# Kernel tuning notes

Hardware: AMD Instinct MI355X
Metric: run time of the kernel (lower is better)

The kernel has to match this reference:

```python
import jax, jax.numpy as jnp
import numpy as np

N = 50000
E = 800000
D = 128
NUM_GRAPHS = 64
NEG_SLOPE = 0.2


def _gat_conv(x, src, dst, W, a_src, a_dst, bias):
    """PyG GATConv with heads=1, concat=True. src/dst include self-loops."""
    h = x @ W                                  # [N, D_out]
    alpha_s = h @ a_src                        # [N]
    alpha_d = h @ a_dst                        # [N]
    e = alpha_s[src] + alpha_d[dst]            # [E_tot] edge scores
    e = jnp.where(e > 0, e, NEG_SLOPE * e)     # LeakyReLU(0.2)
    # numerically-stable softmax over incoming edges of each dst node
    m = jax.ops.segment_max(e, dst, num_segments=N)
    m = jnp.where(jnp.isfinite(m), m, 0.0)
    ex = jnp.exp(e - m[dst])
    s = jax.ops.segment_sum(ex, dst, num_segments=N)
    coef = ex / (s[dst] + 1e-16)               # [E_tot]
    msg = h[src] * coef[:, None]               # [E_tot, D_out] gathered messages
    out = jax.ops.segment_sum(msg, dst, num_segments=N)
    return out + bias


def setup_inputs() -> dict:
    key = jax.random.key(0)
    ks = jax.random.split(key, 12)
    x = jax.random.normal(ks[0], (N, D), dtype=jnp.float32)
    edge_index = jax.random.randint(ks[1], (2, E), 0, N, dtype=jnp.int64)
    batch = jnp.sort(jax.random.randint(ks[2], (N,), 0, NUM_GRAPHS, dtype=jnp.int64))
    g = 1.0 / np.sqrt(D)
    W1 = jax.random.normal(ks[3], (D, D), dtype=jnp.float32) * g
    as1 = jax.random.normal(ks[4], (D,), dtype=jnp.float32) * g
    ad1 = jax.random.normal(ks[5], (D,), dtype=jnp.float32) * g
    b1 = jnp.zeros((D,), dtype=jnp.float32)
    W2 = jax.random.normal(ks[6], (D, D), dtype=jnp.float32) * g
    as2 = jax.random.normal(ks[7], (D,), dtype=jnp.float32) * g
    ad2 = jax.random.normal(ks[8], (D,), dtype=jnp.float32) * g
    b2 = jnp.zeros((D,), dtype=jnp.float32)
    return {"x": x, "edge_index": edge_index, "batch": batch,
            "W1": W1, "as1": as1, "ad1": ad1, "b1": b1,
            "W2": W2, "as2": as2, "ad2": ad2, "b2": b2}


def reference(x, edge_index, batch, W1, as1, ad1, b1, W2, as2, ad2, b2):
    # PyG GATConv adds self-loops by default
    loops = jnp.arange(N, dtype=edge_index.dtype)
    src = jnp.concatenate([edge_index[0], loops])
    dst = jnp.concatenate([edge_index[1], loops])
    feats = _gat_conv(x, src, dst, W1, as1, ad1, b1)
    feats = _gat_conv(feats, src, dst, W2, as2, ad2, b2)
    # global mean pool over graphs in the batch
    sums = jax.ops.segment_sum(feats, batch, num_segments=NUM_GRAPHS)
    counts = jax.ops.segment_sum(jnp.ones((N,), feats.dtype), batch, num_segments=NUM_GRAPHS)
    pooled = sums / jnp.maximum(counts, 1.0)[:, None]
    return feats, pooled
```

## Files before the change

### kernel.cpp

```cpp
#include <hip/hip_runtime.h>

#define NN 50000
#define NE 800000
#define DIM 128
#define NG 64
#define ETOT (NE + NN)
#define NEG_SLOPE 0.2f
#define PB 200
#define MAXLG 8
#define NSH 8
#define SHW ((NN + NSH - 1) / NSH)
#define NB_SCAN ((NN + 255) / 256)

typedef unsigned int uint32;
typedef unsigned short ushort;
typedef short bf16x8 __attribute__((ext_vector_type(8)));
typedef float f32x4 __attribute__((ext_vector_type(4)));

static __device__ __forceinline__ uint32 f2bf_pack(float lo, float hi) {
  uint32 a = __float_as_uint(lo), b = __float_as_uint(hi);
  a = (a + 0x7fffu + ((a >> 16) & 1u)) >> 16;
  b = (b + 0x7fffu + ((b >> 16) & 1u)) >> 16;
  return a | (b << 16);
}
static __device__ __forceinline__ ushort f2bf1(float x) {
  uint32 a = __float_as_uint(x);
  a = (a + 0x7fffu + ((a >> 16) & 1u)) >> 16;
  return (ushort)a;
}
static __device__ __forceinline__ float bf_lo(uint32 u) { return __uint_as_float(u << 16); }
static __device__ __forceinline__ float bf_hi(uint32 u) { return __uint_as_float(u & 0xffff0000u); }


__global__ __launch_bounds__(256) void k_init(const float* __restrict__ W1, const float* __restrict__ W2,
                                              ushort* __restrict__ wt1, ushort* __restrict__ wt2,
                                              int* deg, int* fill, float* pooled, float* cnt) {
  int i = blockIdx.x * 256 + threadIdx.x;
  if (i < NN) { deg[i] = 1; fill[i] = 1; }
  if (i < NG * DIM) pooled[i] = 0.f;
  if (i < NG) cnt[i] = 0.f;
  if (i < DIM * DIM) {
    int n = i >> 7, k = i & 127;
    wt1[i] = f2bf1(W1[k * DIM + n]);
    wt2[i] = f2bf1(W2[k * DIM + n]);
  }
}

__global__ __launch_bounds__(256) void k_count(const int* __restrict__ dst, int* __restrict__ deg) {
  int e = blockIdx.x * 256 + threadIdx.x;
  if (e < NE) atomicAdd(&deg[dst[e]], 1);
}


__global__ __launch_bounds__(256) void k_scan1(const int* __restrict__ deg, int* __restrict__ offs,
                                               int* __restrict__ bsum) {
  __shared__ int ws[4];
  const int i = blockIdx.x * 256 + threadIdx.x;
  const int lane = threadIdx.x & 63, wid = threadIdx.x >> 6;
  int x = (i < NN) ? deg[i] : 0;
#pragma unroll
  for (int off = 1; off < 64; off <<= 1) {
    int t = __shfl_up(x, off, 64);
    if (lane >= off) x += t;
  }
  if (lane == 63) ws[wid] = x;
  __syncthreads();
  int pre = 0;
#pragma unroll
  for (int j = 0; j < 3; ++j) if (j < wid) pre += ws[j];
  x += pre;
  if (i < NN) offs[i + 1] = x;
  if (threadIdx.x == 255) bsum[blockIdx.x] = x;
}

__global__ __launch_bounds__(256) void k_scan2(const int* __restrict__ bsum, int* __restrict__ bpre) {
  __shared__ int ws[4];
  const int b = threadIdx.x;
  const int lane = b & 63, wid = b >> 6;
  int v = (b < NB_SCAN) ? bsum[b] : 0;
  int x = v;
#pragma unroll
  for (int off = 1; off < 64; off <<= 1) {
    int t = __shfl_up(x, off, 64);
    if (lane >= off) x += t;
  }
  if (lane == 63) ws[wid] = x;
  __syncthreads();
  int pre = 0;
#pragma unroll
  for (int j = 0; j < 3; ++j) if (j < wid) pre += ws[j];
  x += pre;
  if (b < NB_SCAN) bpre[b] = x - v;
}

__global__ __launch_bounds__(256) void k_scan3(int* __restrict__ offs, const int* __restrict__ bpre) {
  const int i = blockIdx.x * 256 + threadIdx.x;
  if (i < NN) offs[i + 1] += bpre[blockIdx.x];
  if (i == 0) offs[0] = 0;
}

__global__ __launch_bounds__(256) void k_selfloop(const int* __restrict__ offs, int* __restrict__ csr) {
  int i = blockIdx.x * 256 + threadIdx.x;
  if (i < NN) csr[offs[i]] = i;
}

__global__ __launch_bounds__(256) void k_scatter(const int* __restrict__ src, const int* __restrict__ dst,
                                                 const int* __restrict__ offs, int* __restrict__ fill,
                                                 int* __restrict__ csr) {
  const int r = blockIdx.x & (NSH - 1);
  const int bi = blockIdx.x >> 3;
  const int nb = gridDim.x >> 3;
  const int lo = r * SHW, hi = min(lo + SHW, NN);
  for (int e = bi * 256 + threadIdx.x; e < NE; e += nb * 256) {
    int d = dst[e];
    if (d >= lo && d < hi) {
      int p = offs[d] + atomicAdd(&fill[d], 1);
      csr[p] = src[e];
    }
  }
}


template <int A16>
__global__ __launch_bounds__(256) void k_mm(const void* __restrict__ Xv, const ushort* __restrict__ WT,
                                            const float* __restrict__ a_s, const float* __restrict__ a_d,
                                            uint32* __restrict__ H16,
                                            float* __restrict__ alpha_s, float* __restrict__ alpha_d, int n) {
  __shared__ __align__(16) ushort sWT[DIM * DIM];
  __shared__ __align__(16) ushort sA[64 * DIM];
  const int tid = threadIdx.x;
  const int row0 = blockIdx.x * 64;

  {
    const int nr = tid >> 1, h2 = tid & 1;
    const uint4* wp = (const uint4*)(WT + nr * DIM + h2 * 64);
#pragma unroll
    for (int i = 0; i < 8; ++i) {
      uint4 v = wp[i];
      int byte = nr * 256 + (((h2 * 128 + i * 16)) ^ ((nr & 7) << 4));
      *(uint4*)((char*)sWT + byte) = v;
    }
  }
  {
    const int r = tid >> 2, q = tid & 3;
    int rg = row0 + r; if (rg > n - 1) rg = n - 1;
    if (A16) {
      const uint4* xp = (const uint4*)((const uint32*)Xv + (size_t)rg * 64 + q * 16);
#pragma unroll
      for (int i = 0; i < 4; ++i) {
        uint4 pk = xp[i];
        int byte = r * 256 + ((q * 64 + i * 16) ^ ((r & 7) << 4));
        *(uint4*)((char*)sA + byte) = pk;
      }
    } else {
      const float4* xp = (const float4*)((const float*)Xv + (size_t)rg * DIM + q * 32);
#pragma unroll
      for (int i = 0; i < 4; ++i) {
        float4 v0 = xp[2 * i], v1 = xp[2 * i + 1];
        uint4 pk = make_uint4(f2bf_pack(v0.x, v0.y), f2bf_pack(v0.z, v0.w),
                              f2bf_pack(v1.x, v1.y), f2bf_pack(v1.z, v1.w));
        int byte = r * 256 + ((q * 64 + i * 16) ^ ((r & 7) << 4));
        *(uint4*)((char*)sA + byte) = pk;
      }
    }
  }
  __syncthreads();

  const int l = tid & 63, wv = tid >> 6;
  const int jr = l & 15, g = l >> 4;
  const int m0 = wv * 16;
  f32x4 acc[8];
#pragma unroll
  for (int nt = 0; nt < 8; ++nt) acc[nt] = (f32x4){0.f, 0.f, 0.f, 0.f};

  const int ra = m0 + jr;
  const int abase = ra * 256, aswz = (ra & 7) << 4;
  const int bswz = (jr & 7) << 4;
#pragma unroll
  for (int kk = 0; kk < 4; ++kk) {
    const int kb = kk * 64 + g * 16;
    bf16x8 af = *(const bf16x8*)((const char*)sA + abase + (kb ^ aswz));
#pragma unroll
    for (int nt = 0; nt < 8; ++nt) {
      bf16x8 bfg = *(const bf16x8*)((const char*)sWT + (nt * 16 + jr) * 256 + (kb ^ bswz));
      acc[nt] = __builtin_amdgcn_mfma_f32_16x16x32_bf16(af, bfg, acc[nt], 0, 0, 0);
    }
  }

  float asv[8], adv[8];
#pragma unroll
  for (int nt = 0; nt < 8; ++nt) { asv[nt] = a_s[nt * 16 + jr]; adv[nt] = a_d[nt * 16 + jr]; }
#pragma unroll
  for (int j = 0; j < 4; ++j) {
    float ps = 0.f, pd = 0.f;
#pragma unroll
    for (int nt = 0; nt < 8; ++nt) {
      ps = fmaf(acc[nt][j], asv[nt], ps);
      pd = fmaf(acc[nt][j], adv[nt], pd);
    }
#pragma unroll
    for (int off = 1; off < 16; off <<= 1) {
      ps += __shfl_xor(ps, off, 64);
      pd += __shfl_xor(pd, off, 64);
    }
    int r = row0 + m0 + g * 4 + j;
    if (jr == 0 && r < n) { alpha_s[r] = ps; alpha_d[r] = pd; }
  }

  ushort* sOut = sA;
#pragma unroll
  for (int nt = 0; nt < 8; ++nt)
#pragma unroll
    for (int j = 0; j < 4; ++j)
      sOut[(m0 + g * 4 + j) * DIM + nt * 16 + jr] = f2bf1(acc[nt][j]);
#pragma unroll
  for (int i = 0; i < 4; ++i) {
    int r = row0 + m0 + (l >> 4) + i * 4;
    uint4 v = *(const uint4*)((const char*)sOut + m0 * 256 + l * 16 + i * 1024);
    if (r < n) *(uint4*)(H16 + (size_t)(row0 + m0) * 64 + l * 4 + i * 256) = v;
  }
}


#define GATHER4(J)                                                          \
  { int s0 = __shfl(sv, g32 + (J), 64), s1 = __shfl(sv, g32 + (J) + 1, 64), \
        s2 = __shfl(sv, g32 + (J) + 2, 64), s3 = __shfl(sv, g32 + (J) + 3, 64); \
    float c0 = __shfl(ex, g32 + (J), 64), c1 = __shfl(ex, g32 + (J) + 1, 64), \
          c2 = __shfl(ex, g32 + (J) + 2, 64), c3 = __shfl(ex, g32 + (J) + 3, 64); \
    uint32 v0 = H16[(size_t)s0 * 64 + u0];                                  \
    uint32 v1 = H16[(size_t)s1 * 64 + u0];                                  \
    uint32 v2 = H16[(size_t)s2 * 64 + u0];                                  \
    uint32 v3 = H16[(size_t)s3 * 64 + u0];                                  \
    ax = fmaf(c0, bf_lo(v0), ax); ay = fmaf(c0, bf_hi(v0), ay);             \
    ax = fmaf(c1, bf_lo(v1), ax); ay = fmaf(c1, bf_hi(v1), ay);             \
    ax = fmaf(c2, bf_lo(v2), ax); ay = fmaf(c2, bf_hi(v2), ay);             \
    ax = fmaf(c3, bf_lo(v3), ax); ay = fmaf(c3, bf_hi(v3), ay); }

#define GATHER1(J)                                                          \
  { int s0 = __shfl(sv, g32 + (J), 64); float c0 = __shfl(ex, g32 + (J), 64); \
    uint32 v0 = H16[(size_t)s0 * 64 + u0];                                  \
    ax = fmaf(c0, bf_lo(v0), ax); ay = fmaf(c0, bf_hi(v0), ay); }

template <int STORE16>
__global__ __launch_bounds__(256) void k_sm_aggr2(const int* __restrict__ offs, const int* __restrict__ csr,
                                                  const float* __restrict__ alpha_s, const float* __restrict__ alpha_d,
                                                  const uint32* __restrict__ H16, const float* __restrict__ bias,
                                                  float* __restrict__ out, uint32* __restrict__ out16) {
  const int b = blockIdx.x;
  const int half = b & 1;
  const int l = threadIdx.x & 63;
  const int sl = l & 31, g = l >> 5, g32 = g * 32;
  const int pair = (b >> 1) * 4 + (threadIdx.x >> 6);
  const int node = pair * 2 + g;
  const int bg = offs[node], eg = offs[node + 1];
  const int dg = eg - bg;
  const float ad = alpha_d[node];
  const int u0 = half * 32 + sl;

  const int maxd = max(dg, __shfl_xor(dg, 32, 64));
  float ax = 0.f, ay = 0.f, ssum = 0.f;

  if (maxd <= 32) {
    int sv = 0; float sc = -1e30f;
    if (sl < dg) {
      sv = csr[bg + sl];
      sc = alpha_s[sv] + ad;
      sc = sc > 0.f ? sc : NEG_SLOPE * sc;
    }
    float m = sc;
#pragma unroll
    for (int off = 1; off < 32; off <<= 1) m = fmaxf(m, __shfl_xor(m, off, 64));
    float ex = (sl < dg) ? __expf(sc - m) : 0.f;
    ssum = ex;
    int j = 0;
    for (; j + 3 < maxd; j += 4) GATHER4(j);
    for (; j < maxd; ++j) GATHER1(j);
  } else {
    float m = -1e30f;
    for (int j = sl; j < dg; j += 32) {
      float sc = alpha_s[csr[bg + j]] + ad;
      sc = sc > 0.f ? sc : NEG_SLOPE * sc;
      m = fmaxf(m, sc);
    }
#pragma unroll
    for (int off = 1; off < 32; off <<= 1) m = fmaxf(m, __shfl_xor(m, off, 64));
    const int nch = (maxd + 31) >> 5;
    for (int c = 0; c < nch; ++c) {
      int j = c * 32 + sl;
      int sv = 0; float ex = 0.f;
      if (j < dg) {
        sv = csr[bg + j];
        float sc = alpha_s[sv] + ad;
        sc = sc > 0.f ? sc : NEG_SLOPE * sc;
        ex = __expf(sc - m);
      }
      ssum += ex;
      int cnt = min(32, maxd - c * 32);
      int jj = 0;
      for (; jj + 3 < cnt; jj += 4) GATHER4(jj);
      for (; jj < cnt; ++jj) GATHER1(jj);
    }
  }

#pragma unroll
  for (int off = 1; off < 32; off <<= 1) ssum += __shfl_xor(ssum, off, 64);
  const float inv = 1.f / (ssum + 1e-16f);
  const float2 bb = *(const float2*)(bias + 2 * u0);
  const float ox = ax * inv + bb.x, oy = ay * inv + bb.y;
  if (STORE16) {
    out16[(size_t)node * 64 + u0] = f2bf_pack(ox, oy);
  } else {
    *(float2*)(out + (size_t)node * DIM + 2 * u0) = make_float2(ox, oy);
  }
}


__global__ __launch_bounds__(256) void k_pool_partial(const float* __restrict__ feats,
                                                      const int* __restrict__ batch,
                                                      float* __restrict__ pooled, float* __restrict__ cnt) {
  __shared__ float acc[4][MAXLG][DIM];
  __shared__ float lcnt[4][MAXLG];
  const int tid = threadIdx.x;
  const int wid = tid >> 6, l = tid & 63;
  for (int i = tid; i < 4 * MAXLG * DIM; i += 256) ((float*)acc)[i] = 0.f;
  if (tid < 4 * MAXLG) ((float*)lcnt)[tid] = 0.f;
  __syncthreads();

  const int chunk = (NN + PB - 1) / PB;
  const int beg = blockIdx.x * chunk;
  const int end = min(beg + chunk, NN);
  const int g0 = (beg < NN) ? batch[beg] : 0;

  for (int node = beg + wid; node < end; node += 4) {
    int lg = batch[node] - g0;
    float2 v = *(const float2*)(feats + (size_t)node * DIM + 2 * l);
    if (lg < MAXLG) {
      acc[wid][lg][2 * l] += v.x;
      acc[wid][lg][2 * l + 1] += v.y;
      if (l == 0) lcnt[wid][lg] += 1.f;
    } else {
      atomicAdd(&pooled[(g0 + lg) * DIM + 2 * l], v.x);
      atomicAdd(&pooled[(g0 + lg) * DIM + 2 * l + 1], v.y);
      if (l == 0) atomicAdd(&cnt[g0 + lg], 1.f);
    }
  }
  __syncthreads();

  for (int i = tid; i < MAXLG * DIM; i += 256) {
    int lg = i >> 7, d = i & (DIM - 1);
    float s = acc[0][lg][d] + acc[1][lg][d] + acc[2][lg][d] + acc[3][lg][d];
    if (s != 0.f) atomicAdd(&pooled[(g0 + lg) * DIM + d], s);
  }
  if (tid < MAXLG) {
    float s = lcnt[0][tid] + lcnt[1][tid] + lcnt[2][tid] + lcnt[3][tid];
    if (s != 0.f) atomicAdd(&cnt[g0 + tid], s);
  }
}

__global__ __launch_bounds__(256) void k_pool_norm(float* pooled, const float* __restrict__ cnt) {
  int i = blockIdx.x * 256 + threadIdx.x;
  if (i < NG * DIM) pooled[i] /= fmaxf(cnt[i >> 7], 1.f);
}


static inline size_t pad256(size_t x) { return (x + 255) & ~(size_t)255; }

extern "C" void kernel_launch(void* const* d_in, const int* in_sizes, int n_in,
                              void* d_out, int out_size, void* d_ws, size_t ws_size,
                              hipStream_t stream) {
  const float* x   = (const float*)d_in[0];
  const int* ei    = (const int*)d_in[1];
  const int* batch = (const int*)d_in[2];
  const float* W1  = (const float*)d_in[3];
  const float* as1 = (const float*)d_in[4];
  const float* ad1 = (const float*)d_in[5];
  const float* b1  = (const float*)d_in[6];
  const float* W2  = (const float*)d_in[7];
  const float* as2 = (const float*)d_in[8];
  const float* ad2 = (const float*)d_in[9];
  const float* b2  = (const float*)d_in[10];

  float* out_feats = (float*)d_out;
  float* pooled    = out_feats + (size_t)NN * DIM;

  const int* src = ei;
  const int* dst = ei + NE;

  char* w = (char*)d_ws;
  uint32* h16 = (uint32*)w;   w += pad256((size_t)NN * 64 * 4);
  uint32* f116 = (uint32*)w;  w += pad256((size_t)NN * 64 * 4);
  float* alpha_s = (float*)w; w += pad256((size_t)NN * 4);
  float* alpha_d = (float*)w; w += pad256((size_t)NN * 4);
  int* deg  = (int*)w;        w += pad256((size_t)NN * 4);
  int* offs = (int*)w;        w += pad256((size_t)(NN + 1) * 4);
  int* fill = (int*)w;        w += pad256((size_t)NN * 4);
  int* csr  = (int*)w;        w += pad256((size_t)ETOT * 4);
  float* cnt  = (float*)w;    w += pad256((size_t)NG * 4);
  int* bsum = (int*)w;        w += pad256((size_t)NB_SCAN * 4);
  int* bpre = (int*)w;        w += pad256((size_t)NB_SCAN * 4);
  ushort* wt1 = (ushort*)w;   w += pad256((size_t)DIM * DIM * 2);
  ushort* wt2 = (ushort*)w;   w += pad256((size_t)DIM * DIM * 2);

  const int NB_N = (NN + 255) / 256;
  const int NB_E = (NE + 255) / 256;
  const int NB_A = (NN / 2 / 4) * 2;
  const int NB_G = (NN + 63) / 64;
  const int NB_SC = 1024;

  k_init<<<NB_N, 256, 0, stream>>>(W1, W2, wt1, wt2, deg, fill, pooled, cnt);
  k_count<<<NB_E, 256, 0, stream>>>(dst, deg);
  k_scan1<<<NB_SCAN, 256, 0, stream>>>(deg, offs, bsum);
  k_scan2<<<1, 256, 0, stream>>>(bsum, bpre);
  k_scan3<<<NB_SCAN, 256, 0, stream>>>(offs, bpre);
  k_selfloop<<<NB_N, 256, 0, stream>>>(offs, csr);
  k_scatter<<<NB_SC, 256, 0, stream>>>(src, dst, offs, fill, csr);

  k_mm<0><<<NB_G, 256, 0, stream>>>(x, wt1, as1, ad1, h16, alpha_s, alpha_d, NN);
  k_sm_aggr2<1><<<NB_A, 256, 0, stream>>>(offs, csr, alpha_s, alpha_d, h16, b1, nullptr, f116);

  k_mm<1><<<NB_G, 256, 0, stream>>>(f116, wt2, as2, ad2, h16, alpha_s, alpha_d, NN);
  k_sm_aggr2<0><<<NB_A, 256, 0, stream>>>(offs, csr, alpha_s, alpha_d, h16, b2, out_feats, nullptr);

  k_pool_partial<<<PB, 256, 0, stream>>>(out_feats, batch, pooled, cnt);
  k_pool_norm<<<(NG * DIM + 255) / 256, 256, 0, stream>>>(pooled, cnt);
}
```

Before: 220.3 us.

## Restructure GAT aggregation to stage edges and softmax weights per 64-node block in LDS

Replaces the per-node-pair aggregation kernel with a block-per-64-nodes kernel. It first loads all incoming edge sources and alpha_s values into shared memory, then computes the softmax max, exp and sum cooperatively (16 lanes per node), then runs the gather with one full wave per node reading indices and weights from LDS instead of shuffles. A global-memory fallback handles blocks with more than 2048 edges. The self-loop insertion is also folded into the scan3 kernel, removing one launch. The cost is extra synchronisations and LDS use, which may lower occupancy.

```diff
diff --git a/kernel.cpp b/kernel.cpp
--- a/kernel.cpp
+++ b/kernel.cpp
@@ -11,6 +11,7 @@
 #define NSH 8
 #define SHW ((NN + NSH - 1) / NSH)
 #define NB_SCAN ((NN + 255) / 256)
+#define CAP 2048
 
 typedef unsigned int uint32;
 typedef unsigned short ushort;
@@ -93,15 +94,15 @@
   if (b < NB_SCAN) bpre[b] = x - v;
 }
 
-__global__ __launch_bounds__(256) void k_scan3(int* __restrict__ offs, const int* __restrict__ bpre) {
+__global__ __launch_bounds__(256) void k_scan3(int* __restrict__ offs, const int* __restrict__ bpre,
+                                               const int* __restrict__ deg, int* __restrict__ csr) {
   const int i = blockIdx.x * 256 + threadIdx.x;
-  if (i < NN) offs[i + 1] += bpre[blockIdx.x];
+  if (i < NN) {
+    int v = offs[i + 1] + bpre[blockIdx.x];
+    offs[i + 1] = v;
+    csr[v - deg[i]] = i;
+  }
   if (i == 0) offs[0] = 0;
-}
-
-__global__ __launch_bounds__(256) void k_selfloop(const int* __restrict__ offs, int* __restrict__ csr) {
-  int i = blockIdx.x * 256 + threadIdx.x;
-  if (i < NN) csr[offs[i]] = i;
 }
 
 __global__ __launch_bounds__(256) void k_scatter(const int* __restrict__ src, const int* __restrict__ dst,
@@ -222,95 +223,123 @@
 }
 
 
-#define GATHER4(J)                                                          \
-  { int s0 = __shfl(sv, g32 + (J), 64), s1 = __shfl(sv, g32 + (J) + 1, 64), \
-        s2 = __shfl(sv, g32 + (J) + 2, 64), s3 = __shfl(sv, g32 + (J) + 3, 64); \
-    float c0 = __shfl(ex, g32 + (J), 64), c1 = __shfl(ex, g32 + (J) + 1, 64), \
-          c2 = __shfl(ex, g32 + (J) + 2, 64), c3 = __shfl(ex, g32 + (J) + 3, 64); \
-    uint32 v0 = H16[(size_t)s0 * 64 + u0];                                  \
-    uint32 v1 = H16[(size_t)s1 * 64 + u0];                                  \
-    uint32 v2 = H16[(size_t)s2 * 64 + u0];                                  \
-    uint32 v3 = H16[(size_t)s3 * 64 + u0];                                  \
-    ax = fmaf(c0, bf_lo(v0), ax); ay = fmaf(c0, bf_hi(v0), ay);             \
-    ax = fmaf(c1, bf_lo(v1), ax); ay = fmaf(c1, bf_hi(v1), ay);             \
-    ax = fmaf(c2, bf_lo(v2), ax); ay = fmaf(c2, bf_hi(v2), ay);             \
-    ax = fmaf(c3, bf_lo(v3), ax); ay = fmaf(c3, bf_hi(v3), ay); }
-
-#define GATHER1(J)                                                          \
-  { int s0 = __shfl(sv, g32 + (J), 64); float c0 = __shfl(ex, g32 + (J), 64); \
-    uint32 v0 = H16[(size_t)s0 * 64 + u0];                                  \
-    ax = fmaf(c0, bf_lo(v0), ax); ay = fmaf(c0, bf_hi(v0), ay); }
-
 template <int STORE16>
-__global__ __launch_bounds__(256) void k_sm_aggr2(const int* __restrict__ offs, const int* __restrict__ csr,
-                                                  const float* __restrict__ alpha_s, const float* __restrict__ alpha_d,
-                                                  const uint32* __restrict__ H16, const float* __restrict__ bias,
-                                                  float* __restrict__ out, uint32* __restrict__ out16) {
-  const int b = blockIdx.x;
-  const int half = b & 1;
-  const int l = threadIdx.x & 63;
-  const int sl = l & 31, g = l >> 5, g32 = g * 32;
-  const int pair = (b >> 1) * 4 + (threadIdx.x >> 6);
-  const int node = pair * 2 + g;
-  const int bg = offs[node], eg = offs[node + 1];
-  const int dg = eg - bg;
-  const float ad = alpha_d[node];
-  const int u0 = half * 32 + sl;
-
-  const int maxd = max(dg, __shfl_xor(dg, 32, 64));
-  float ax = 0.f, ay = 0.f, ssum = 0.f;
-
-  if (maxd <= 32) {
-    int sv = 0; float sc = -1e30f;
-    if (sl < dg) {
-      sv = csr[bg + sl];
-      sc = alpha_s[sv] + ad;
-      sc = sc > 0.f ? sc : NEG_SLOPE * sc;
-    }
-    float m = sc;
-#pragma unroll
-    for (int off = 1; off < 32; off <<= 1) m = fmaxf(m, __shfl_xor(m, off, 64));
-    float ex = (sl < dg) ? __expf(sc - m) : 0.f;
-    ssum = ex;
-    int j = 0;
-    for (; j + 3 < maxd; j += 4) GATHER4(j);
-    for (; j < maxd; ++j) GATHER1(j);
+__global__ __launch_bounds__(256) void k_sma(const int* __restrict__ offs, const int* __restrict__ csr,
+                                             const float* __restrict__ alpha_s, const float* __restrict__ alpha_d,
+                                             const uint32* __restrict__ H16, const float* __restrict__ bias,
+                                             float* __restrict__ out, uint32* __restrict__ out16) {
+  __shared__ int s_src[CAP];
+  __shared__ float s_ex[CAP];
+  __shared__ float s_inv[64];
+  __shared__ int s_off[65];
+  const int tid = threadIdx.x;
+  const int n0 = blockIdx.x * 64;
+  const int nn = min(64, NN - n0);
+  if (tid <= nn) s_off[tid] = offs[n0 + tid];
+  __syncthreads();
+  const int ebeg = s_off[0];
+  const int nE = s_off[nn] - ebeg;
+  const int l = tid & 63, wv = tid >> 6;
+  const float2 bb = *(const float2*)(bias + 2 * l);
+
+  if (nE <= CAP) {
+    for (int e = tid; e < nE; e += 256) {
+      int sv = csr[ebeg + e];
+      s_src[e] = sv;
+      s_ex[e] = alpha_s[sv];
+    }
+    __syncthreads();
+    {
+      const int g = tid >> 4, l16 = tid & 15;
+      for (int i = g; i < nn; i += 16) {
+        const float ad = alpha_d[n0 + i];
+        const int jb = s_off[i] - ebeg, je = s_off[i + 1] - ebeg;
+        float m = -1e30f;
+        for (int j = jb + l16; j < je; j += 16) {
+          float sc = s_ex[j] + ad;
+          sc = sc > 0.f ? sc : NEG_SLOPE * sc;
+          m = fmaxf(m, sc);
+        }
+#pragma unroll
+        for (int off = 1; off < 16; off <<= 1) m = fmaxf(m, __shfl_xor(m, off, 64));
+        float ssum = 0.f;
+        for (int j = jb + l16; j < je; j += 16) {
+          float sc = s_ex[j] + ad;
+          sc = sc > 0.f ? sc : NEG_SLOPE * sc;
+          float ex = __expf(sc - m);
+          s_ex[j] = ex;
+          ssum += ex;
+        }
+#pragma unroll
+        for (int off = 1; off < 16; off <<= 1) ssum += __shfl_xor(ssum, off, 64);
+        if (l16 == 0) s_inv[i] = 1.f / (ssum + 1e-16f);
+      }
+    }
+    __syncthreads();
+    for (int i = wv; i < nn; i += 4) {
+      const int jb = s_off[i] - ebeg, je = s_off[i + 1] - ebeg;
+      float ax = 0.f, ay = 0.f;
+      int j = jb;
+      for (; j + 3 < je; j += 4) {
+        int s0 = s_src[j], s1 = s_src[j + 1], s2 = s_src[j + 2], s3 = s_src[j + 3];
+        float c0 = s_ex[j], c1 = s_ex[j + 1], c2 = s_ex[j + 2], c3 = s_ex[j + 3];
+        uint32 v0 = H16[(size_t)s0 * 64 + l];
+        uint32 v1 = H16[(size_t)s1 * 64 + l];
+        uint32 v2 = H16[(size_t)s2 * 64 + l];
+        uint32 v3 = H16[(size_t)s3 * 64 + l];
+        ax = fmaf(c0, bf_lo(v0), ax); ay = fmaf(c0, bf_hi(v0), ay);
+        ax = fmaf(c1, bf_lo(v1), ax); ay = fmaf(c1, bf_hi(v1), ay);
+        ax = fmaf(c2, bf_lo(v2), ax); ay = fmaf(c2, bf_hi(v2), ay);
+        ax = fmaf(c3, bf_lo(v3), ax); ay = fmaf(c3, bf_hi(v3), ay);
+      }
+      for (; j < je; ++j) {
+        int s0 = s_src[j]; float c0 = s_ex[j];
+        uint32 v0 = H16[(size_t)s0 * 64 + l];
+        ax = fmaf(c0, bf_lo(v0), ax); ay = fmaf(c0, bf_hi(v0), ay);
+      }
+      const float inv = s_inv[i];
+      const float ox = ax * inv + bb.x, oy = ay * inv + bb.y;
+      const int node = n0 + i;
+      if (STORE16) out16[(size_t)node * 64 + l] = f2bf_pack(ox, oy);
+      else *(float2*)(out + (size_t)node * DIM + 2 * l) = make_float2(ox, oy);
+    }
   } else {
-    float m = -1e30f;
-    for (int j = sl; j < dg; j += 32) {
-      float sc = alpha_s[csr[bg + j]] + ad;
-      sc = sc > 0.f ? sc : NEG_SLOPE * sc;
-      m = fmaxf(m, sc);
-    }
-#pragma unroll
-    for (int off = 1; off < 32; off <<= 1) m = fmaxf(m, __shfl_xor(m, off, 64));
-    const int nch = (maxd + 31) >> 5;
-    for (int c = 0; c < nch; ++c) {
-      int j = c * 32 + sl;
-      int sv = 0; float ex = 0.f;
-      if (j < dg) {
-        sv = csr[bg + j];
-        float sc = alpha_s[sv] + ad;
+    for (int i = wv; i < nn; i += 4) {
+      const int node = n0 + i;
+      const int bg = offs[node], eg = offs[node + 1];
+      const float ad = alpha_d[node];
+      float m = -1e30f;
+      for (int jj = bg + l; jj < eg; jj += 64) {
+        float sc = alpha_s[csr[jj]] + ad;
         sc = sc > 0.f ? sc : NEG_SLOPE * sc;
-        ex = __expf(sc - m);
-      }
-      ssum += ex;
-      int cnt = min(32, maxd - c * 32);
-      int jj = 0;
-      for (; jj + 3 < cnt; jj += 4) GATHER4(jj);
-      for (; jj < cnt; ++jj) GATHER1(jj);
-    }
-  }
-
-#pragma unroll
-  for (int off = 1; off < 32; off <<= 1) ssum += __shfl_xor(ssum, off, 64);
-  const float inv = 1.f / (ssum + 1e-16f);
-  const float2 bb = *(const float2*)(bias + 2 * u0);
-  const float ox = ax * inv + bb.x, oy = ay * inv + bb.y;
-  if (STORE16) {
-    out16[(size_t)node * 64 + u0] = f2bf_pack(ox, oy);
-  } else {
-    *(float2*)(out + (size_t)node * DIM + 2 * u0) = make_float2(ox, oy);
+        m = fmaxf(m, sc);
+      }
+#pragma unroll
+      for (int off = 1; off < 64; off <<= 1) m = fmaxf(m, __shfl_xor(m, off, 64));
+      float ax = 0.f, ay = 0.f, ssum = 0.f;
+      for (int base = bg; base < eg; base += 64) {
+        int cnt = min(64, eg - base);
+        int sv = 0; float ex = 0.f;
+        if (l < cnt) {
+          sv = csr[base + l];
+          float sc = alpha_s[sv] + ad;
+          sc = sc > 0.f ? sc : NEG_SLOPE * sc;
+          ex = __expf(sc - m);
+        }
+        ssum += ex;
+        for (int jj = 0; jj < cnt; ++jj) {
+          int s0 = __shfl(sv, jj, 64); float c0 = __shfl(ex, jj, 64);
+          uint32 v0 = H16[(size_t)s0 * 64 + l];
+          ax = fmaf(c0, bf_lo(v0), ax); ay = fmaf(c0, bf_hi(v0), ay);
+        }
+      }
+#pragma unroll
+      for (int off = 1; off < 64; off <<= 1) ssum += __shfl_xor(ssum, off, 64);
+      const float inv = 1.f / (ssum + 1e-16f);
+      const float ox = ax * inv + bb.x, oy = ay * inv + bb.y;
+      if (STORE16) out16[(size_t)node * 64 + l] = f2bf_pack(ox, oy);
+      else *(float2*)(out + (size_t)node * DIM + 2 * l) = make_float2(ox, oy);
+    }
   }
 }
 
@@ -403,7 +432,7 @@
 
   const int NB_N = (NN + 255) / 256;
   const int NB_E = (NE + 255) / 256;
-  const int NB_A = (NN / 2 / 4) * 2;
+  const int NB_A = (NN + 63) / 64;
   const int NB_G = (NN + 63) / 64;
   const int NB_SC = 1024;
 
@@ -411,15 +440,14 @@
   k_count<<<NB_E, 256, 0, stream>>>(dst, deg);
   k_scan1<<<NB_SCAN, 256, 0, stream>>>(deg, offs, bsum);
   k_scan2<<<1, 256, 0, stream>>>(bsum, bpre);
-  k_scan3<<<NB_SCAN, 256, 0, stream>>>(offs, bpre);
-  k_selfloop<<<NB_N, 256, 0, stream>>>(offs, csr);
+  k_scan3<<<NB_SCAN, 256, 0, stream>>>(offs, bpre, deg, csr);
   k_scatter<<<NB_SC, 256, 0, stream>>>(src, dst, offs, fill, csr);
 
   k_mm<0><<<NB_G, 256, 0, stream>>>(x, wt1, as1, ad1, h16, alpha_s, alpha_d, NN);
-  k_sm_aggr2<1><<<NB_A, 256, 0, stream>>>(offs, csr, alpha_s, alpha_d, h16, b1, nullptr, f116);
+  k_sma<1><<<NB_A, 256, 0, stream>>>(offs, csr, alpha_s, alpha_d, h16, b1, nullptr, f116);
 
   k_mm<1><<<NB_G, 256, 0, stream>>>(f116, wt2, as2, ad2, h16, alpha_s, alpha_d, NN);
-  k_sm_aggr2<0><<<NB_A, 256, 0, stream>>>(offs, csr, alpha_s, alpha_d, h16, b2, out_feats, nullptr);
+  k_sma<0><<<NB_A, 256, 0, stream>>>(offs, csr, alpha_s, alpha_d, h16, b2, out_feats, nullptr);
 
   k_pool_partial<<<PB, 256, 0, stream>>>(out_feats, batch, pooled, cnt);
   k_pool_norm<<<(NG * DIM + 255) / 256, 256, 0, stream>>>(pooled, cnt);
```

New measurement: 248.0 us. +12.6%, slower.
